# Optimization experiments

Hardware: AMD Instinct MI355X
Metric: run time of the kernel (lower is better)

Reference implementation:

```python
import jax, jax.numpy as jnp
import numpy as np
from jax import lax


def _fps(xyz, num_group):
    """Farthest point sampling. xyz: (B, N, 3) -> centers (B, G, 3).
    Sequential over G (structural loop) via lax.scan; starts at index 0."""
    B, N, _ = xyz.shape

    def step(carry, _):
        min_d, last_idx = carry                      # (B, N), (B,)
        last_pt = jax.vmap(lambda p, i: p[i])(xyz, last_idx)  # (B, 3)
        d = jnp.sum((xyz - last_pt[:, None, :]) ** 2, axis=-1)  # (B, N)
        min_d = jnp.minimum(min_d, d)
        nxt = jnp.argmax(min_d, axis=-1).astype(jnp.int32)
        return (min_d, nxt), last_idx

    init = (jnp.full((B, N), jnp.inf, dtype=xyz.dtype),
            jnp.zeros((B,), dtype=jnp.int32))
    _, idxs = lax.scan(step, init, None, length=num_group)  # (G, B)
    idxs = idxs.T                                            # (B, G)
    centers = jax.vmap(lambda p, i: p[i])(xyz, idxs)         # (B, G, 3)
    return centers


def setup_inputs() -> dict:
    key = jax.random.key(0)
    xyz = jax.random.normal(key, (32, 8192, 3), dtype=jnp.float32)
    return {"xyz": xyz, "num_group": 256, "group_size": 32}


def reference(xyz, num_group, group_size):
    B, N, C = xyz.shape
    center = _fps(xyz, num_group)                            # (B, G, 3)
    # dense pairwise distances: (B, G, N)
    dist = jnp.linalg.norm(center[:, :, None, :] - xyz[:, None, :, :], axis=-1)
    _, idx = lax.top_k(-dist, group_size)                    # (B, G, k) smallest dists
    # gather neighbors per batch: (B, G, k, 3)
    patch = jax.vmap(lambda pts, i: pts[i])(xyz, idx)
    patch = patch - center[:, :, None, :]                    # recenter
    return (patch, center)
```

## Files before the change

### kernel.cpp

```cpp
#include <hip/hip_runtime.h>

#pragma clang fp contract(off)

#define BB 32
#define NN 8192
#define GG 256
#define KK 32

#define TFPS 512
#define JPF (NN / TFPS)

template <int CTRL>
__device__ __forceinline__ float rot_maxf(float v) {
  const int o =
      __builtin_amdgcn_update_dpp(0, __float_as_int(v), CTRL, 0xF, 0xF, true);
  return fmaxf(v, __int_as_float(o));
}

__global__ __launch_bounds__(TFPS, 1) void fps_kernel(const float* __restrict__ xyz,
                                                      float* __restrict__ out) {
#pragma clang fp contract(off)
  const int b = blockIdx.x;
  const int t = threadIdx.x;
  const int lane = t & 63;
  const int wave = t >> 6;
  const float* __restrict__ P = xyz + (size_t)b * NN * 3;

  __shared__ float4 pts[NN];
  __shared__ float rowmax[2][32];
  __shared__ unsigned winIdx[2];

  float px[JPF], py[JPF], pz[JPF], md[JPF];
#pragma unroll
  for (int j = 0; j < JPF; ++j) {
    const int idx = t + j * TFPS;
    const float x = P[idx * 3 + 0];
    const float y = P[idx * 3 + 1];
    const float z = P[idx * 3 + 2];
    px[j] = x; py[j] = y; pz[j] = z;
    md[j] = __builtin_inff();
    pts[idx] = make_float4(x, y, z, 0.0f);
  }
  if (t == 0) { winIdx[0] = 0xFFFFFFFFu; winIdx[1] = 0xFFFFFFFFu; }
  __syncthreads();

  unsigned win = 0;
  unsigned mywin = 0;

  for (int i = 0; i < GG; ++i) {
    if (t == i) mywin = win;
    if (i == GG - 1) break;

    const float4 c = pts[win];
    const float cx = c.x, cy = c.y, cz = c.z;

    float bv = -1.0f;
#pragma unroll
    for (int j = 0; j < JPF; ++j) {
      const float dx = px[j] - cx;
      const float dy = py[j] - cy;
      const float dz = pz[j] - cz;
      const float d = dx * dx + dy * dy + dz * dz;
      const float m = md[j] < d ? md[j] : d;
      md[j] = m;
      bv = fmaxf(bv, m);
    }

    float r = bv;
    r = rot_maxf<0x121>(r);
    r = rot_maxf<0x122>(r);
    r = rot_maxf<0x124>(r);
    r = rot_maxf<0x128>(r);
    if ((lane & 15) == 0)
      rowmax[i & 1][wave * 4 + (lane >> 4)] = r;
    __syncthreads();

    if (t == 0) winIdx[(i + 1) & 1] = 0xFFFFFFFFu;

    const float* __restrict__ rm = rowmax[i & 1];
    const int g = lane & 15;
    float m2 = fmaxf(rm[g], rm[g + 16]);
    m2 = rot_maxf<0x121>(m2);
    m2 = rot_maxf<0x122>(m2);
    m2 = rot_maxf<0x124>(m2);
    m2 = rot_maxf<0x128>(m2);
    const float M = m2;

    if (bv == M) {
      int fj = 0;
#pragma unroll
      for (int j = JPF - 1; j >= 0; --j)
        if (md[j] == M) fj = j;
      atomicMin(&winIdx[i & 1], (unsigned)t + ((unsigned)fj << 9));
    }
    __syncthreads();

    win = winIdx[i & 1];
  }

  if (t < GG) {
    const float4 c = pts[mywin];
    float* __restrict__ co =
        out + (size_t)BB * GG * KK * 3 + ((size_t)b * GG + t) * 3;
    co[0] = c.x; co[1] = c.y; co[2] = c.z;
  }
}

__global__ __launch_bounds__(512, 1) void knn_kernel(const float* __restrict__ xyz,
                                                     float* __restrict__ out) {
#pragma clang fp contract(off)
  const int b = blockIdx.x >> 3;
  const int chunk = blockIdx.x & 7;
  const int t = threadIdx.x;
  const int lane = t & 63;
  const int wave = t >> 6;
  const float* __restrict__ P = xyz + (size_t)b * NN * 3;

  __shared__ float4 pts4[NN];
  __shared__ unsigned long long cand[8][256];

  for (int pt = t; pt < NN; pt += 512)
    pts4[pt] = make_float4(P[pt * 3 + 0], P[pt * 3 + 1], P[pt * 3 + 2], 0.0f);
  __syncthreads();

  const float* __restrict__ cent = out + (size_t)BB * GG * KK * 3;
  const int gbase = chunk * 32 + wave * 4;

  const float c0x = cent[((size_t)b * GG + gbase + 0) * 3 + 0];
  const float c0y = cent[((size_t)b * GG + gbase + 0) * 3 + 1];
  const float c0z = cent[((size_t)b * GG + gbase + 0) * 3 + 2];
  const float c1x = cent[((size_t)b * GG + gbase + 1) * 3 + 0];
  const float c1y = cent[((size_t)b * GG + gbase + 1) * 3 + 1];
  const float c1z = cent[((size_t)b * GG + gbase + 1) * 3 + 2];
  const float c2x = cent[((size_t)b * GG + gbase + 2) * 3 + 0];
  const float c2y = cent[((size_t)b * GG + gbase + 2) * 3 + 1];
  const float c2z = cent[((size_t)b * GG + gbase + 2) * 3 + 2];
  const float c3x = cent[((size_t)b * GG + gbase + 3) * 3 + 0];
  const float c3y = cent[((size_t)b * GG + gbase + 3) * 3 + 1];
  const float c3z = cent[((size_t)b * GG + gbase + 3) * 3 + 2];

  float mn0 = __builtin_inff(), mn1 = __builtin_inff();
  float mn2 = __builtin_inff(), mn3 = __builtin_inff();
#pragma unroll 4
  for (int j = 0; j < 128; ++j) {
    const float4 p = pts4[lane + j * 64];
    {
      const float dx = p.x - c0x, dy = p.y - c0y, dz = p.z - c0z;
      mn0 = fminf(mn0, dx * dx + dy * dy + dz * dz);
    }
    {
      const float dx = p.x - c1x, dy = p.y - c1y, dz = p.z - c1z;
      mn1 = fminf(mn1, dx * dx + dy * dy + dz * dz);
    }
    {
      const float dx = p.x - c2x, dy = p.y - c2y, dz = p.z - c2z;
      mn2 = fminf(mn2, dx * dx + dy * dy + dz * dz);
    }
    {
      const float dx = p.x - c3x, dy = p.y - c3y, dz = p.z - c3z;
      mn3 = fminf(mn3, dx * dx + dy * dy + dz * dz);
    }
  }

  auto thresh = [&](float mn) -> float {
    float sm = mn;
#pragma unroll
    for (int k = 2; k <= 64; k <<= 1) {
#pragma unroll
      for (int j2 = k >> 1; j2 > 0; j2 >>= 1) {
        const float o = __shfl_xor(sm, j2, 64);
        const bool keepMin = (((lane & k) == 0) == ((lane & j2) == 0));
        sm = keepMin ? fminf(sm, o) : fmaxf(sm, o);
      }
    }
    const float v = __shfl(sm, 31, 64);
    return __uint_as_float(__float_as_uint(v) + 8);
  };
  const float vi0 = thresh(mn0);
  const float vi1 = thresh(mn1);
  const float vi2 = thresh(mn2);
  const float vi3 = thresh(mn3);

  auto dogroup = [&](int g, float cx, float cy, float cz, float vi) {
    unsigned cnt = 0;
    unsigned long long* __restrict__ cb = cand[wave];
#pragma unroll 4
    for (int j = 0; j < 128; ++j) {
      const int idx = lane + j * 64;
      const float4 p = pts4[idx];
      const float dx = p.x - cx, dy = p.y - cy, dz = p.z - cz;
      const float d2 = dx * dx + dy * dy + dz * dz;
      const bool pr = d2 <= vi;
      const unsigned long long mk = __ballot(pr);
      if (pr) {
        const unsigned off = cnt + (unsigned)__popcll(mk & ((1ull << lane) - 1));
        if (off < 256)
          cb[off] = ((unsigned long long)__float_as_uint(d2) << 32) |
                    (unsigned)idx;
      }
      cnt += (unsigned)__popcll(mk);
    }
    if (cnt > 256) cnt = 256;

    auto conv = [](unsigned long long e) -> unsigned long long {
      const float d = sqrtf(__uint_as_float((unsigned)(e >> 32)));
      return ((unsigned long long)__float_as_uint(d) << 32) | (e & 0xFFFFFFFFull);
    };

    unsigned long long myk;
    if (cnt <= 64) {
      unsigned long long key = ~0ull;
      if ((unsigned)lane < cnt) key = conv(cb[lane]);
#pragma unroll
      for (int k = 2; k <= 64; k <<= 1) {
#pragma unroll
        for (int j2 = k >> 1; j2 > 0; j2 >>= 1) {
          const unsigned long long o = __shfl_xor(key, j2, 64);
          const bool keepMin = (((lane & k) == 0) == ((lane & j2) == 0));
          const unsigned long long lo = o < key ? o : key;
          const unsigned long long hi = o < key ? key : o;
          key = keepMin ? lo : hi;
        }
      }
      myk = key;
    } else {
      unsigned long long k0 = ~0ull, k1 = ~0ull, k2 = ~0ull, k3 = ~0ull;
      if ((unsigned)lane < cnt)         k0 = conv(cb[lane]);
      if ((unsigned)(lane + 64) < cnt)  k1 = conv(cb[lane + 64]);
      if ((unsigned)(lane + 128) < cnt) k2 = conv(cb[lane + 128]);
      if ((unsigned)(lane + 192) < cnt) k3 = conv(cb[lane + 192]);
      unsigned long long got = ~0ull;
      for (int r = 0; r < 32; ++r) {
        unsigned long long m01 = k0 < k1 ? k0 : k1;
        unsigned long long m23 = k2 < k3 ? k2 : k3;
        unsigned long long m = m01 < m23 ? m01 : m23;
#pragma unroll
        for (int s = 32; s > 0; s >>= 1) {
          const unsigned long long o = __shfl_xor(m, s, 64);
          m = o < m ? o : m;
        }
        if (lane == r) got = m;
        if (k0 == m) k0 = ~0ull;
        else if (k1 == m) k1 = ~0ull;
        else if (k2 == m) k2 = ~0ull;
        else if (k3 == m) k3 = ~0ull;
      }
      myk = got;
    }

    if (lane < KK) {
      const unsigned idx = (unsigned)(myk & 0xFFFFFFFFull);
      const float4 p = pts4[idx];
      float* __restrict__ po =
          out + ((size_t)(((size_t)b * GG + g) * KK + lane)) * 3;
      po[0] = p.x - cx; po[1] = p.y - cy; po[2] = p.z - cz;
    }
  };

  dogroup(gbase + 0, c0x, c0y, c0z, vi0);
  dogroup(gbase + 1, c1x, c1y, c1z, vi1);
  dogroup(gbase + 2, c2x, c2y, c2z, vi2);
  dogroup(gbase + 3, c3x, c3y, c3z, vi3);
}

extern "C" void kernel_launch(void* const* d_in, const int* in_sizes, int n_in,
                              void* d_out, int out_size, void* d_ws, size_t ws_size,
                              hipStream_t stream) {
  const float* xyz = (const float*)d_in[0];
  float* out = (float*)d_out;
  fps_kernel<<<dim3(BB), dim3(TFPS), 0, stream>>>(xyz, out);
  knn_kernel<<<dim3(BB * 8), dim3(512), 0, stream>>>(xyz, out);
}
```

Baseline: 319.2 us.

## Carry winner coordinates through DPP argmax and cut FPS to one barrier

The farthest-point-sampling kernel is restructured so the argmax reduction carries the winning point's coordinates alongside the distance. This removes the shared point array, the atomicMin winner-index pass and the second barrier in each iteration. Each 1024-thread block now processes two batches, one per half, and each half finishes its reduction with DPP over per-wave slots. The goal is shorter per-iteration latency in the sequential 255-step loop. The trade-off is that tie-breaking between equal distances may no longer always pick the lowest point index.

```diff
diff --git a/kernel.cpp b/kernel.cpp
--- a/kernel.cpp
+++ b/kernel.cpp
@@ -7,53 +7,65 @@
 #define GG 256
 #define KK 32
 
-#define TFPS 512
-#define JPF (NN / TFPS)
+#define TB 1024
+#define TPB 512
+#define JPF 16
 
 template <int CTRL>
-__device__ __forceinline__ float rot_maxf(float v) {
+__device__ __forceinline__ float dppmax_f(float v) {
   const int o =
       __builtin_amdgcn_update_dpp(0, __float_as_int(v), CTRL, 0xF, 0xF, true);
   return fmaxf(v, __int_as_float(o));
 }
 
-__global__ __launch_bounds__(TFPS, 1) void fps_kernel(const float* __restrict__ xyz,
-                                                      float* __restrict__ out) {
+template <int CTRL>
+__device__ __forceinline__ float4 red_stage(float4 e) {
+  float4 o;
+  o.x = __int_as_float(
+      __builtin_amdgcn_update_dpp(0, __float_as_int(e.x), CTRL, 0xF, 0xF, true));
+  o.y = __int_as_float(
+      __builtin_amdgcn_update_dpp(0, __float_as_int(e.y), CTRL, 0xF, 0xF, true));
+  o.z = __int_as_float(
+      __builtin_amdgcn_update_dpp(0, __float_as_int(e.z), CTRL, 0xF, 0xF, true));
+  o.w = __int_as_float(
+      __builtin_amdgcn_update_dpp(0, __float_as_int(e.w), CTRL, 0xF, 0xF, true));
+  const bool gt = __float_as_uint(o.w) > __float_as_uint(e.w);
+  float4 r;
+  r.x = gt ? o.x : e.x;
+  r.y = gt ? o.y : e.y;
+  r.z = gt ? o.z : e.z;
+  r.w = gt ? o.w : e.w;
+  return r;
+}
+
+__global__ __launch_bounds__(TB) void fps_kernel(const float* __restrict__ xyz,
+                                                 float* __restrict__ out) {
 #pragma clang fp contract(off)
-  const int b = blockIdx.x;
   const int t = threadIdx.x;
   const int lane = t & 63;
   const int wave = t >> 6;
-  const float* __restrict__ P = xyz + (size_t)b * NN * 3;
-
-  __shared__ float4 pts[NN];
-  __shared__ float rowmax[2][32];
-  __shared__ unsigned winIdx[2];
+  const int h = wave >> 3;
+  const int tb = t & (TPB - 1);
+  const int batch = blockIdx.x * 2 + h;
+  const float* __restrict__ P = xyz + (size_t)batch * NN * 3;
+
+  __shared__ float4 wslot[2][16];
 
   float px[JPF], py[JPF], pz[JPF], md[JPF];
 #pragma unroll
   for (int j = 0; j < JPF; ++j) {
-    const int idx = t + j * TFPS;
-    const float x = P[idx * 3 + 0];
-    const float y = P[idx * 3 + 1];
-    const float z = P[idx * 3 + 2];
-    px[j] = x; py[j] = y; pz[j] = z;
+    const int idx = tb + j * TPB;
+    px[j] = P[idx * 3 + 0];
+    py[j] = P[idx * 3 + 1];
+    pz[j] = P[idx * 3 + 2];
     md[j] = __builtin_inff();
-    pts[idx] = make_float4(x, y, z, 0.0f);
-  }
-  if (t == 0) { winIdx[0] = 0xFFFFFFFFu; winIdx[1] = 0xFFFFFFFFu; }
-  __syncthreads();
-
-  unsigned win = 0;
-  unsigned mywin = 0;
-
-  for (int i = 0; i < GG; ++i) {
-    if (t == i) mywin = win;
-    if (i == GG - 1) break;
-
-    const float4 c = pts[win];
-    const float cx = c.x, cy = c.y, cz = c.z;
-
+  }
+
+  float cx = P[0], cy = P[1], cz = P[2];
+  float sx = 0.f, sy = 0.f, sz = 0.f;
+  if (tb == 0) { sx = cx; sy = cy; sz = cz; }
+
+  for (int i = 0; i < GG - 1; ++i) {
     float bv = -1.0f;
 #pragma unroll
     for (int j = 0; j < JPF; ++j) {
@@ -66,43 +78,41 @@
       bv = fmaxf(bv, m);
     }
 
-    float r = bv;
-    r = rot_maxf<0x121>(r);
-    r = rot_maxf<0x122>(r);
-    r = rot_maxf<0x124>(r);
-    r = rot_maxf<0x128>(r);
-    if ((lane & 15) == 0)
-      rowmax[i & 1][wave * 4 + (lane >> 4)] = r;
+    float v = bv;
+    v = dppmax_f<0x121>(v);
+    v = dppmax_f<0x122>(v);
+    v = dppmax_f<0x124>(v);
+    v = dppmax_f<0x128>(v);
+    v = dppmax_f<0x142>(v);
+    v = dppmax_f<0x143>(v);
+    const unsigned Mw =
+        (unsigned)__builtin_amdgcn_readlane(__float_as_int(v), 63);
+
+    const bool cand = (__float_as_uint(bv) == Mw);
+    const unsigned long long bal = __ballot(cand);
+    const int wl = __ffsll((long long)bal) - 1;
+    if (lane == wl) {
+      float wx = px[0], wy = py[0], wz = pz[0];
+#pragma unroll
+      for (int j = JPF - 1; j >= 0; --j) {
+        if (__float_as_uint(md[j]) == Mw) { wx = px[j]; wy = py[j]; wz = pz[j]; }
+      }
+      wslot[i & 1][wave] = make_float4(wx, wy, wz, __uint_as_float(Mw));
+    }
     __syncthreads();
 
-    if (t == 0) winIdx[(i + 1) & 1] = 0xFFFFFFFFu;
-
-    const float* __restrict__ rm = rowmax[i & 1];
-    const int g = lane & 15;
-    float m2 = fmaxf(rm[g], rm[g + 16]);
-    m2 = rot_maxf<0x121>(m2);
-    m2 = rot_maxf<0x122>(m2);
-    m2 = rot_maxf<0x124>(m2);
-    m2 = rot_maxf<0x128>(m2);
-    const float M = m2;
-
-    if (bv == M) {
-      int fj = 0;
-#pragma unroll
-      for (int j = JPF - 1; j >= 0; --j)
-        if (md[j] == M) fj = j;
-      atomicMin(&winIdx[i & 1], (unsigned)t + ((unsigned)fj << 9));
-    }
-    __syncthreads();
-
-    win = winIdx[i & 1];
-  }
-
-  if (t < GG) {
-    const float4 c = pts[mywin];
+    float4 e = wslot[i & 1][h * 8 + (lane & 7)];
+    e = red_stage<0x121>(e);
+    e = red_stage<0x122>(e);
+    e = red_stage<0x124>(e);
+    cx = e.x; cy = e.y; cz = e.z;
+    if (tb == i + 1) { sx = cx; sy = cy; sz = cz; }
+  }
+
+  if (tb < GG) {
     float* __restrict__ co =
-        out + (size_t)BB * GG * KK * 3 + ((size_t)b * GG + t) * 3;
-    co[0] = c.x; co[1] = c.y; co[2] = c.z;
+        out + (size_t)BB * GG * KK * 3 + ((size_t)batch * GG + tb) * 3;
+    co[0] = sx; co[1] = sy; co[2] = sz;
   }
 }
 
@@ -268,6 +278,6 @@
                               hipStream_t stream) {
   const float* xyz = (const float*)d_in[0];
   float* out = (float*)d_out;
-  fps_kernel<<<dim3(BB), dim3(TFPS), 0, stream>>>(xyz, out);
+  fps_kernel<<<dim3(BB / 2), dim3(TB), 0, stream>>>(xyz, out);
   knn_kernel<<<dim3(BB * 8), dim3(512), 0, stream>>>(xyz, out);
 }
```

Measured after the change: 590.1 us. 1.85x slower.
